# Kernel tuning notes

Hardware: AMD Instinct MI355X
Metric: run time of the kernel (lower is better)

## Reference

```python
import jax, jax.numpy as jnp
import numpy as np

B = 512        # number of graphs
NPG = 128      # nodes per graph
N = B * NPG    # total nodes = 65536
E = 262144     # total edges (intra-graph)
F_IN = 128     # input features
H = 256        # hidden
C = 2          # num classes
BN_EPS = 1e-5


def _lin_params(key, fan_in, fan_out):
    k1, k2 = jax.random.split(key)
    s = 1.0 / np.sqrt(fan_in)
    w = jax.random.uniform(k1, (fan_in, fan_out), jnp.float32, -s, s)
    b = jax.random.uniform(k2, (fan_out,), jnp.float32, -s, s)
    return w, b


def setup_inputs() -> dict:
    key = jax.random.key(0)
    ks = jax.random.split(key, 16)
    x = jax.random.normal(ks[0], (N, F_IN), jnp.float32)
    # intra-graph random edges (required for assignment pooling semantics)
    rng = np.random.RandomState(0)
    g = np.repeat(np.arange(B), E // B)
    src = g * NPG + rng.randint(0, NPG, E)
    dst = g * NPG + rng.randint(0, NPG, E)
    edge_index = jnp.asarray(np.stack([src, dst]), jnp.int64 if jax.config.jax_enable_x64 else jnp.int32)
    batch = jnp.repeat(jnp.arange(B), NPG)
    # GIN layer 0 (F_IN->H->H) + BN
    w0_1, b0_1 = _lin_params(ks[1], F_IN, H)
    w0_2, b0_2 = _lin_params(ks[2], H, H)
    g0 = jnp.ones((H,), jnp.float32); be0 = jnp.zeros((H,), jnp.float32)
    # GIN layers 1..2 stacked (H->H->H) + BN
    wl1 = jnp.stack([_lin_params(jax.random.fold_in(ks[3], i), H, H)[0] for i in range(2)])
    bl1 = jnp.stack([_lin_params(jax.random.fold_in(ks[3], i), H, H)[1] for i in range(2)])
    wl2 = jnp.stack([_lin_params(jax.random.fold_in(ks[4], i), H, H)[0] for i in range(2)])
    bl2 = jnp.stack([_lin_params(jax.random.fold_in(ks[4], i), H, H)[1] for i in range(2)])
    gl = jnp.ones((2, H), jnp.float32); bel = jnp.zeros((2, H), jnp.float32)
    c1w, c1b = _lin_params(ks[5], H, H)
    c2w, c2b = _lin_params(ks[6], H, 2)
    l1w, l1b = _lin_params(ks[7], H, H)
    l2w, l2b = _lin_params(ks[8], H, C)
    return dict(x=x, edge_index=edge_index, batch=batch,
                w0_1=w0_1, b0_1=b0_1, w0_2=w0_2, b0_2=b0_2, g0=g0, be0=be0,
                wl1=wl1, bl1=bl1, wl2=wl2, bl2=bl2, gl=gl, bel=bel,
                c1w=c1w, c1b=c1b, c2w=c2w, c2b=c2b,
                l1w=l1w, l1b=l1b, l2w=l2w, l2b=l2b)


def _gin_layer(h, src, dst, w1, b1, w2, b2, gamma, beta):
    # GINConv (eps=0): MLP(h + sum_{j in N(i)} h_j)
    agg = jax.ops.segment_sum(h[src], dst, num_segments=N)
    z = h + agg
    z = jax.nn.relu(z @ w1 + b1)
    z = jax.nn.relu(z @ w2 + b2)
    # BatchNorm1d, training-mode batch stats (biased variance)
    mu = jnp.mean(z, axis=0)
    var = jnp.mean((z - mu) ** 2, axis=0)
    return (z - mu) * jax.lax.rsqrt(var + BN_EPS) * gamma + beta


def reference(x, edge_index, batch, w0_1, b0_1, w0_2, b0_2, g0, be0,
              wl1, bl1, wl2, bl2, gl, bel,
              c1w, c1b, c2w, c2b, l1w, l1b, l2w, l2b):
    src, dst = edge_index[0], edge_index[1]
    h = _gin_layer(x, src, dst, w0_1, b0_1, w0_2, b0_2, g0, be0)
    for i in range(2):
        h = _gin_layer(h, src, dst, wl1[i], bl1[i], wl2[i], bl2[i], gl[i], bel[i])
    # assignment: softmax(cluster2(tanh(cluster1(h))))  -> [N, 2]
    a = jax.nn.softmax(jnp.tanh(h @ c1w + c1b) @ c2w + c2b, axis=1)
    # subgraph embedding: (assignment^T @ x)[0] per graph == segment-sum of a[:,0]*h
    sub = jax.ops.segment_sum(a[:, :1] * h, batch, num_segments=B)        # [B, H]
    # graph embedding: per-graph mean of h
    cnt = jax.ops.segment_sum(jnp.ones((N,), h.dtype), batch, num_segments=B)
    graph = jax.ops.segment_sum(h, batch, num_segments=B) / cnt[:, None]   # [B, H]
    # new_adj[g] = A_g^T-pooled: sum over edges outer(a[src], a[dst]) -> [B,2,2]
    new_adj = jax.ops.segment_sum(a[src][:, :, None] * a[dst][:, None, :], batch[src], num_segments=B)
    # F.normalize(p=1, dim=1) row-wise, then diagonal, MSE vs ones(2)
    rown = jnp.maximum(jnp.sum(jnp.abs(new_adj), axis=2, keepdims=True), 1e-12)
    norm_adj = new_adj / rown
    diag = jnp.diagonal(norm_adj, axis1=1, axis2=2)                        # [B, 2]
    con_penalty = jnp.mean(jnp.mean((diag - 1.0) ** 2, axis=1))
    # classifier head (dropout in eval mode -> identity)
    z = jax.nn.relu(sub @ l1w + l1b)
    out = jax.nn.log_softmax(z @ l2w + l2b, axis=-1)
    return out, sub, graph, con_penalty
```

## Files before the change

### kernel.cpp

```cpp
#include <hip/hip_runtime.h>
#include <stdint.h>

#define NN 65536
#define NB 512
#define NPG 128
#define NE 262144
#define EPG 512
#define HD 256
#define BN_EPS 1e-5f

typedef unsigned short u16;
typedef float f32x4 __attribute__((ext_vector_type(4)));
typedef __bf16 bf16x8 __attribute__((ext_vector_type(8)));
typedef unsigned short u16x8 __attribute__((ext_vector_type(8)));
typedef unsigned short u16x4 __attribute__((ext_vector_type(4)));

__device__ __forceinline__ float b2f(u16 u){
  union { unsigned i; float f; } x; x.i = ((unsigned)u) << 16; return x.f;
}
__device__ __forceinline__ u16 f2b(float f){
  union { float f; unsigned i; } x; x.f = f;
  unsigned r = x.i + 0x7fffu + ((x.i >> 16) & 1u);
  return (u16)(r >> 16);
}

__global__ void __launch_bounds__(256) pack_all(
    const float* __restrict__ w0_1, const float* __restrict__ w0_2,
    const float* __restrict__ wl1, const float* __restrict__ wl2,
    const float* __restrict__ c1w,
    u16* i01, u16* i02, u16* il1a, u16* il1b, u16* il2a, u16* il2b, u16* ic1)
{
  const int seg = blockIdx.y;
  const int idx = blockIdx.x * 256 + threadIdx.x;
  const float* W; u16* img; int K = 256;
  switch (seg){
    case 0: W = w0_1;        img = i01;  K = 128; break;
    case 1: W = w0_2;        img = i02;  break;
    case 2: W = wl1;         img = il1a; break;
    case 3: W = wl1 + 65536; img = il1b; break;
    case 4: W = wl2;         img = il2a; break;
    case 5: W = wl2 + 65536; img = il2b; break;
    default: W = c1w;        img = ic1;  break;
  }
  if (idx >= K * 256) return;
  int col = idx / K, k = idx - col * K;
  img[idx] = f2b(W[(size_t)k * 256 + col]);
}

template<int K>
__device__ __forceinline__ void mm_frag(const u16* Alds,
    const u16* __restrict__ wimg, int lane, int c0, f32x4 (&acc)[8][2])
{
  const int l15 = lane & 15, lk = (lane >> 4) * 8;
  bf16x8 bfr[K / 32][2];
  #pragma unroll
  for (int kk = 0; kk < K / 32; kk++)
    #pragma unroll
    for (int nf = 0; nf < 2; nf++)
      bfr[kk][nf] = *(const bf16x8*)(wimg + (size_t)(c0 + nf * 16 + l15) * K + kk * 32 + lk);
  #pragma unroll
  for (int kk = 0; kk < K / 32; kk++){
    bf16x8 af[8];
    #pragma unroll
    for (int mf = 0; mf < 8; mf++){
      int row = mf * 16 + l15;
      unsigned byte = ((unsigned)(row * (K * 2) + (kk * 32 + lk) * 2)) ^ (unsigned)((row & 7) << 4);
      af[mf] = *(const bf16x8*)((const char*)Alds + byte);
    }
    #pragma unroll
    for (int mf = 0; mf < 8; mf++)
      #pragma unroll
      for (int nf = 0; nf < 2; nf++)
        acc[mf][nf] = __builtin_amdgcn_mfma_f32_16x16x32_bf16(af[mf], bfr[kk][nf], acc[mf][nf], 0, 0, 0);
  }
}

template<int KIN, int MODE>
__global__ void __launch_bounds__(512) layer_kernel(
    const void* __restrict__ hin_, const int* __restrict__ ei,
    const float* __restrict__ sc, const float* __restrict__ sh,
    const u16* __restrict__ w1img, const float* __restrict__ b1,
    const u16* __restrict__ w2img, const float* __restrict__ b2,
    u16* __restrict__ Y, float* __restrict__ pS, float* __restrict__ pQ)
{
  __shared__ u16 ht[NPG * KIN];
  __shared__ u16 z1[NPG * HD];
  __shared__ int es[EPG], ed[EPG], srcs[EPG];
  __shared__ int cnt[NPG], rp[NPG + 1], fill[NPG];
  __shared__ float scs[256], shs[256];
  const int g = blockIdx.x, tid = threadIdx.x;
  const int lane = tid & 63, wid = tid >> 6;

  if (tid < NPG) cnt[tid] = 0;
  if (MODE == 1 && tid < 256){ scs[tid] = sc[tid]; shs[tid] = sh[tid]; }
  __syncthreads();

  {
    int s = ei[g * EPG + tid] & (NPG - 1);
    int d = ei[NE + g * EPG + tid] & (NPG - 1);
    es[tid] = s; ed[tid] = d;
    atomicAdd(&cnt[d], 1);
  }

  if constexpr (MODE == 0){
    const float* hin = (const float*)hin_;
    #pragma unroll
    for (int i = 0; i < 8; i++){
      int idx = tid + i * 512;
      int row = idx >> 5, c4 = idx & 31;
      float4 v = *(const float4*)(hin + (size_t)(g * NPG + row) * KIN + c4 * 4);
      u16x4 o; o[0] = f2b(v.x); o[1] = f2b(v.y); o[2] = f2b(v.z); o[3] = f2b(v.w);
      unsigned byte = ((unsigned)(row * (KIN * 2) + c4 * 8)) ^ (unsigned)((row & 7) << 4);
      *(u16x4*)((char*)ht + byte) = o;
    }
  } else {
    const u16* hin = (const u16*)hin_;
    #pragma unroll
    for (int i = 0; i < 8; i++){
      int idx = tid + i * 512;
      int row = idx >> 5, c8 = idx & 31;
      u16x8 v = *(const u16x8*)(hin + (size_t)(g * NPG + row) * KIN + c8 * 8);
      u16x8 o;
      #pragma unroll
      for (int k = 0; k < 8; k++) o[k] = f2b(b2f(v[k]) * scs[c8 * 8 + k] + shs[c8 * 8 + k]);
      unsigned byte = ((unsigned)(row * (KIN * 2) + c8 * 16)) ^ (unsigned)((row & 7) << 4);
      *(u16x8*)((char*)ht + byte) = o;
    }
  }
  __syncthreads();

  if (tid < 64){
    int a = cnt[tid], b = cnt[tid + 64];
    int ca = a, cb = b;
    #pragma unroll
    for (int off = 1; off < 64; off <<= 1){
      int ta = __shfl_up(a, off), tb = __shfl_up(b, off);
      if (lane >= off){ a += ta; b += tb; }
    }
    int atot = __shfl(a, 63);
    rp[tid + 1] = a;
    rp[tid + 65] = atot + b;
    fill[tid] = a - ca;
    fill[tid + 64] = atot + b - cb;
    if (tid == 0) rp[0] = 0;
  }
  __syncthreads();
  { int pos = atomicAdd(&fill[ed[tid]], 1); srcs[pos] = es[tid]; }
  __syncthreads();

  constexpr int CH = KIN / 16;
  constexpr int RPT = NPG * CH / 512;
  const int fc = tid & (CH - 1), n0 = tid / CH;
  float accv[RPT][16];
  #pragma unroll
  for (int j = 0; j < RPT; j++){
    const int n = n0 + j * (512 / CH);
    unsigned b0 = ((unsigned)(n * (KIN * 2) + fc * 32)) ^ (unsigned)((n & 7) << 4);
    u16x8 a0 = *(const u16x8*)((const char*)ht + b0);
    u16x8 a1 = *(const u16x8*)((const char*)ht + (b0 ^ 16u));
    #pragma unroll
    for (int k = 0; k < 8; k++){ accv[j][k] = b2f(a0[k]); accv[j][8 + k] = b2f(a1[k]); }
    const int e0 = rp[n], e1 = rp[n + 1];
    for (int e = e0; e < e1; e++){
      const int sn = srcs[e];
      unsigned s0 = ((unsigned)(sn * (KIN * 2) + fc * 32)) ^ (unsigned)((sn & 7) << 4);
      u16x8 q0 = *(const u16x8*)((const char*)ht + s0);
      u16x8 q1 = *(const u16x8*)((const char*)ht + (s0 ^ 16u));
      #pragma unroll
      for (int k = 0; k < 8; k++){ accv[j][k] += b2f(q0[k]); accv[j][8 + k] += b2f(q1[k]); }
    }
  }
  __syncthreads();
  #pragma unroll
  for (int j = 0; j < RPT; j++){
    const int n = n0 + j * (512 / CH);
    u16x8 o0, o1;
    #pragma unroll
    for (int k = 0; k < 8; k++){ o0[k] = f2b(accv[j][k]); o1[k] = f2b(accv[j][8 + k]); }
    unsigned b0 = ((unsigned)(n * (KIN * 2) + fc * 32)) ^ (unsigned)((n & 7) << 4);
    *(u16x8*)((char*)ht + b0) = o0;
    *(u16x8*)((char*)ht + (b0 ^ 16u)) = o1;
  }
  __syncthreads();

  const int c0 = wid * 32;
  const int l15 = lane & 15;
  {
    f32x4 acc1[8][2] = {};
    mm_frag<KIN>(ht, w1img, lane, c0, acc1);
    float bv0 = b1[c0 + l15], bv1 = b1[c0 + 16 + l15];
    #pragma unroll
    for (int mf = 0; mf < 8; mf++)
      #pragma unroll
      for (int nf = 0; nf < 2; nf++){
        float bv = nf ? bv1 : bv0;
        int col = c0 + nf * 16 + l15;
        #pragma unroll
        for (int j = 0; j < 4; j++){
          int row = mf * 16 + (lane >> 4) * 4 + j;
          float v = fmaxf(acc1[mf][nf][j] + bv, 0.f);
          unsigned byte = ((unsigned)(row * 512 + col * 2)) ^ (unsigned)((row & 7) << 4);
          *(u16*)((char*)z1 + byte) = f2b(v);
        }
      }
  }
  __syncthreads();

  {
    f32x4 acc2[8][2] = {};
    mm_frag<HD>(z1, w2img, lane, c0, acc2);
    float bv0 = b2[c0 + l15], bv1 = b2[c0 + 16 + l15];
    float s[2] = {0, 0}, q[2] = {0, 0};
    #pragma unroll
    for (int mf = 0; mf < 8; mf++)
      #pragma unroll
      for (int nf = 0; nf < 2; nf++){
        float bv = nf ? bv1 : bv0;
        int col = c0 + nf * 16 + l15;
        #pragma unroll
        for (int j = 0; j < 4; j++){
          int row = mf * 16 + (lane >> 4) * 4 + j;
          float v = fmaxf(acc2[mf][nf][j] + bv, 0.f);
          Y[(size_t)(g * NPG + row) * HD + col] = f2b(v);
          s[nf] += v; q[nf] += v * v;
        }
      }
    #pragma unroll
    for (int nf = 0; nf < 2; nf++){
      float sv = s[nf], qv = q[nf];
      sv += __shfl_xor(sv, 16); sv += __shfl_xor(sv, 32);
      qv += __shfl_xor(qv, 16); qv += __shfl_xor(qv, 32);
      if (lane < 16){
        int col = c0 + nf * 16 + lane;
        pS[(size_t)col * NB + g] = sv;
        pQ[(size_t)col * NB + g] = qv;
      }
    }
  }
}

__global__ void __launch_bounds__(64) bnfin_kernel(const float* __restrict__ pS,
    const float* __restrict__ pQ, const float* __restrict__ gma,
    const float* __restrict__ bta, float* __restrict__ scale, float* __restrict__ shift)
{
  int c = blockIdx.x, lane = threadIdx.x;
  float s = 0.f, q = 0.f;
  for (int i = lane; i < NB; i += 64){ s += pS[(size_t)c * NB + i]; q += pQ[(size_t)c * NB + i]; }
  for (int m = 32; m; m >>= 1){ s += __shfl_xor(s, m); q += __shfl_xor(q, m); }
  if (lane == 0){
    float mu = s * (1.0f / NN);
    float var = q * (1.0f / NN) - mu * mu;
    float scv = gma[c] * rsqrtf(var + BN_EPS);
    scale[c] = scv;
    shift[c] = bta[c] - mu * scv;
  }
}

__global__ void __launch_bounds__(512) final_kernel(
    const u16* __restrict__ hin, const int* __restrict__ ei,
    const float* __restrict__ sc, const float* __restrict__ sh,
    const u16* __restrict__ c1img, const float* __restrict__ c1b,
    const float* __restrict__ c2w, const float* __restrict__ c2b,
    const float* __restrict__ l1w, const float* __restrict__ l1b,
    const float* __restrict__ l2w, const float* __restrict__ l2b,
    float* __restrict__ outLog, float* __restrict__ outSub,
    float* __restrict__ outGraph, float* __restrict__ pg)
{
  __shared__ u16 ht[NPG * HD];
  __shared__ u16 tt[NPG * HD];
  __shared__ int es[EPG], ed[EPG];
  __shared__ float aL[NPG * 2];
  __shared__ float c2ws[512];
  __shared__ float scs[256], shs[256];
  __shared__ float red2[1024];
  __shared__ float subL[256];
  __shared__ float wred[8][4];
  const int g = blockIdx.x, tid = threadIdx.x;
  const int lane = tid & 63, wid = tid >> 6;

  if (tid < 256){ scs[tid] = sc[tid]; shs[tid] = sh[tid]; }
  c2ws[tid] = c2w[tid];
  es[tid] = ei[g * EPG + tid] & (NPG - 1);
  ed[tid] = ei[NE + g * EPG + tid] & (NPG - 1);
  __syncthreads();

  #pragma unroll
  for (int i = 0; i < 8; i++){
    int idx = tid + i * 512;
    int row = idx >> 5, c8 = idx & 31;
    u16x8 v = *(const u16x8*)(hin + (size_t)(g * NPG + row) * HD + c8 * 8);
    u16x8 o;
    #pragma unroll
    for (int k = 0; k < 8; k++) o[k] = f2b(b2f(v[k]) * scs[c8 * 8 + k] + shs[c8 * 8 + k]);
    unsigned byte = ((unsigned)(row * 512 + c8 * 16)) ^ (unsigned)((row & 7) << 4);
    *(u16x8*)((char*)ht + byte) = o;
  }
  __syncthreads();

  const int c0 = wid * 32;
  const int l15 = lane & 15;
  {
    f32x4 acct[8][2] = {};
    mm_frag<HD>(ht, c1img, lane, c0, acct);
    float bv0 = c1b[c0 + l15], bv1 = c1b[c0 + 16 + l15];
    #pragma unroll
    for (int mf = 0; mf < 8; mf++)
      #pragma unroll
      for (int nf = 0; nf < 2; nf++){
        float bv = nf ? bv1 : bv0;
        int col = c0 + nf * 16 + l15;
        #pragma unroll
        for (int j = 0; j < 4; j++){
          int row = mf * 16 + (lane >> 4) * 4 + j;
          tt[row * HD + col] = f2b(tanhf(acct[mf][nf][j] + bv));
        }
      }
  }
  __syncthreads();

  {
    const int n = tid >> 2, qd = tid & 3;
    float s0 = 0.f, s1 = 0.f;
    #pragma unroll
    for (int i = 0; i < 8; i++){
      u16x8 v = *(const u16x8*)&tt[n * HD + qd * 64 + i * 8];
      #pragma unroll
      for (int k = 0; k < 8; k++){
        float f = b2f(v[k]); int col = qd * 64 + i * 8 + k;
        s0 += f * c2ws[col * 2]; s1 += f * c2ws[col * 2 + 1];
      }
    }
    s0 += __shfl_xor(s0, 1); s0 += __shfl_xor(s0, 2);
    s1 += __shfl_xor(s1, 1); s1 += __shfl_xor(s1, 2);
    if (qd == 0){
      s0 += c2b[0]; s1 += c2b[1];
      float mx = fmaxf(s0, s1);
      float e0 = expf(s0 - mx), e1 = expf(s1 - mx);
      float inv = 1.f / (e0 + e1);
      aL[n * 2] = e0 * inv; aL[n * 2 + 1] = e1 * inv;
    }
  }
  __syncthreads();

  {
    float as0 = aL[es[tid] * 2], as1 = aL[es[tid] * 2 + 1];
    float ad0 = aL[ed[tid] * 2], ad1 = aL[ed[tid] * 2 + 1];
    float m00 = as0 * ad0, m01 = as0 * ad1, m10 = as1 * ad0, m11 = as1 * ad1;
    #pragma unroll
    for (int m = 1; m < 64; m <<= 1){
      m00 += __shfl_xor(m00, m); m01 += __shfl_xor(m01, m);
      m10 += __shfl_xor(m10, m); m11 += __shfl_xor(m11, m);
    }
    if (lane == 0){ wred[wid][0] = m00; wred[wid][1] = m01; wred[wid][2] = m10; wred[wid][3] = m11; }
  }
  {
    const int part = tid >> 8, c = tid & 255;
    float sb = 0.f, gs = 0.f;
    #pragma unroll 8
    for (int i = 0; i < 64; i++){
      int n = part * 64 + i;
      unsigned byte = ((unsigned)(n * 512 + c * 2)) ^ (unsigned)((n & 7) << 4);
      float v = b2f(*(const u16*)((const char*)ht + byte));
      sb += aL[n * 2] * v; gs += v;
    }
    red2[part * 512 + c] = sb;
    red2[part * 512 + 256 + c] = gs;
  }
  __syncthreads();
  if (tid < 256){
    float sb = red2[tid] + red2[512 + tid];
    float gs = red2[256 + tid] + red2[768 + tid];
    subL[tid] = sb;
    outSub[(size_t)g * HD + tid] = sb;
    outGraph[(size_t)g * HD + tid] = gs * (1.f / NPG);
  }
  if (tid == 0){
    float m00 = 0, m01 = 0, m10 = 0, m11 = 0;
    for (int w = 0; w < 8; w++){ m00 += wred[w][0]; m01 += wred[w][1]; m10 += wred[w][2]; m11 += wred[w][3]; }
    float r0 = fmaxf(fabsf(m00) + fabsf(m01), 1e-12f);
    float r1 = fmaxf(fabsf(m10) + fabsf(m11), 1e-12f);
    float d0 = m00 / r0 - 1.f, d1 = m11 / r1 - 1.f;
    pg[g] = 0.5f * (d0 * d0 + d1 * d1);
  }
  __syncthreads();

  {
    const int ph = tid >> 8, c = tid & 255;
    float z = 0.f;
    for (int k = ph * 128; k < ph * 128 + 128; k++)
      z += subL[k] * l1w[(size_t)k * HD + c];
    red2[ph * 256 + c] = z;
  }
  __syncthreads();
  if (tid < 256){
    float z = fmaxf(red2[tid] + red2[256 + tid] + l1b[tid], 0.f);
    float o0 = z * l2w[tid * 2], o1 = z * l2w[tid * 2 + 1];
    #pragma unroll
    for (int m = 1; m < 64; m <<= 1){ o0 += __shfl_xor(o0, m); o1 += __shfl_xor(o1, m); }
    if (lane == 0){ wred[wid][0] = o0; wred[wid][1] = o1; }
  }
  __syncthreads();
  if (tid == 0){
    float o0 = wred[0][0] + wred[1][0] + wred[2][0] + wred[3][0] + l2b[0];
    float o1 = wred[0][1] + wred[1][1] + wred[2][1] + wred[3][1] + l2b[1];
    float mx = fmaxf(o0, o1);
    float lse = mx + logf(expf(o0 - mx) + expf(o1 - mx));
    outLog[(size_t)g * 2] = o0 - lse;
    outLog[(size_t)g * 2 + 1] = o1 - lse;
  }
}

__global__ void __launch_bounds__(256) penred_kernel(const float* __restrict__ pg,
                                                     float* __restrict__ outPen)
{
  const int tid = threadIdx.x;
  float s = pg[tid] + pg[tid + 256];
  for (int m = 32; m; m >>= 1) s += __shfl_xor(s, m);
  __shared__ float wsum[4];
  if ((tid & 63) == 0) wsum[tid >> 6] = s;
  __syncthreads();
  if (tid == 0) outPen[0] = (wsum[0] + wsum[1] + wsum[2] + wsum[3]) * (1.0f / NB);
}

extern "C" void kernel_launch(void* const* d_in, const int* in_sizes, int n_in,
                              void* d_out, int out_size, void* d_ws, size_t ws_size,
                              hipStream_t stream)
{
  (void)in_sizes; (void)n_in; (void)out_size; (void)ws_size;
  const float* x    = (const float*)d_in[0];
  const int*   ei   = (const int*)  d_in[1];
  const float* w0_1 = (const float*)d_in[3];
  const float* b0_1 = (const float*)d_in[4];
  const float* w0_2 = (const float*)d_in[5];
  const float* b0_2 = (const float*)d_in[6];
  const float* g0   = (const float*)d_in[7];
  const float* be0  = (const float*)d_in[8];
  const float* wl1  = (const float*)d_in[9];
  const float* bl1  = (const float*)d_in[10];
  const float* wl2  = (const float*)d_in[11];
  const float* bl2  = (const float*)d_in[12];
  const float* gl   = (const float*)d_in[13];
  const float* bel  = (const float*)d_in[14];
  const float* c1w  = (const float*)d_in[15];
  const float* c1b  = (const float*)d_in[16];
  const float* c2w  = (const float*)d_in[17];
  const float* c2b  = (const float*)d_in[18];
  const float* l1w  = (const float*)d_in[19];
  const float* l1b  = (const float*)d_in[20];
  const float* l2w  = (const float*)d_in[21];
  const float* l2b  = (const float*)d_in[22];
  float* out = (float*)d_out;

  char* cur = (char*)d_ws;
  auto carve = [&](size_t bytes) -> void* {
    void* p = (void*)cur; cur += (bytes + 255) & ~(size_t)255; return p;
  };
  u16* B0    = (u16*)carve((size_t)NN * HD * 2);
  u16* B1    = (u16*)carve((size_t)NN * HD * 2);
  u16* i01   = (u16*)carve((size_t)128 * 256 * 2);
  u16* i02   = (u16*)carve((size_t)256 * 256 * 2);
  u16* il1a  = (u16*)carve((size_t)256 * 256 * 2);
  u16* il1b  = (u16*)carve((size_t)256 * 256 * 2);
  u16* il2a  = (u16*)carve((size_t)256 * 256 * 2);
  u16* il2b  = (u16*)carve((size_t)256 * 256 * 2);
  u16* ic1   = (u16*)carve((size_t)256 * 256 * 2);
  float* pS  = (float*)carve((size_t)256 * NB * 4);
  float* pQ  = (float*)carve((size_t)256 * NB * 4);
  float* bsc = (float*)carve(256 * 4);
  float* bsh = (float*)carve(256 * 4);
  float* pg  = (float*)carve(NB * 4);

  pack_all<<<dim3(256, 7), 256, 0, stream>>>(w0_1, w0_2, wl1, wl2, c1w,
                                             i01, i02, il1a, il1b, il2a, il2b, ic1);

  layer_kernel<128, 0><<<NB, 512, 0, stream>>>((const void*)x, ei, nullptr, nullptr,
                                               i01, b0_1, i02, b0_2, B0, pS, pQ);
  bnfin_kernel<<<256, 64, 0, stream>>>(pS, pQ, g0, be0, bsc, bsh);

  layer_kernel<256, 1><<<NB, 512, 0, stream>>>((const void*)B0, ei, bsc, bsh,
                                               il1a, bl1, il2a, bl2, B1, pS, pQ);
  bnfin_kernel<<<256, 64, 0, stream>>>(pS, pQ, gl, bel, bsc, bsh);

  layer_kernel<256, 1><<<NB, 512, 0, stream>>>((const void*)B1, ei, bsc, bsh,
                                               il1b, bl1 + 256, il2b, bl2 + 256, B0, pS, pQ);
  bnfin_kernel<<<256, 64, 0, stream>>>(pS, pQ, gl + 256, bel + 256, bsc, bsh);

  final_kernel<<<NB, 512, 0, stream>>>(B0, ei, bsc, bsh, ic1, c1b, c2w, c2b,
                                       l1w, l1b, l2w, l2b,
                                       out, out + 1024, out + 1024 + NB * HD, pg);
  penred_kernel<<<1, 256, 0, stream>>>(pg, out + 1024 + 2 * NB * HD);
}
```

Before: 309.4 us.

## Cut shared memory in layer and final kernels, fuse cluster head, drop penalty kernel

The layer kernel now reuses the ht buffer for the first MLP output instead of a separate z1 buffer, and packs source and destination edge indices into 16-bit values. Together these shrink LDS use per block so more blocks can be resident per CU. The final kernel fuses the tanh and c2 projection into the MFMA epilogue using a fast exp-based tanh and lane shuffles, which removes the tt buffer and folds the small scratch arrays into one. The separate penalty-reduction kernel is replaced by a float atomicAdd after a memset. The cost is an extra barrier, a less accurate tanh, and a penalty sum whose order is nondeterministic.

```diff
diff --git a/kernel.cpp b/kernel.cpp
--- a/kernel.cpp
+++ b/kernel.cpp
@@ -22,6 +22,10 @@
   union { float f; unsigned i; } x; x.f = f;
   unsigned r = x.i + 0x7fffu + ((x.i >> 16) & 1u);
   return (u16)(r >> 16);
+}
+__device__ __forceinline__ float ftanh(float x){
+  float e = __expf(2.0f * x);
+  return 1.0f - 2.0f * __builtin_amdgcn_rcpf(e + 1.0f);
 }
 
 __global__ void __launch_bounds__(256) pack_all(
@@ -83,9 +87,9 @@
     const u16* __restrict__ w2img, const float* __restrict__ b2,
     u16* __restrict__ Y, float* __restrict__ pS, float* __restrict__ pQ)
 {
-  __shared__ u16 ht[NPG * KIN];
-  __shared__ u16 z1[NPG * HD];
-  __shared__ int es[EPG], ed[EPG], srcs[EPG];
+  __shared__ u16 ht[NPG * HD];
+  __shared__ u16 esd[EPG];
+  __shared__ u16 srcs[EPG];
   __shared__ int cnt[NPG], rp[NPG + 1], fill[NPG];
   __shared__ float scs[256], shs[256];
   const int g = blockIdx.x, tid = threadIdx.x;
@@ -98,7 +102,7 @@
   {
     int s = ei[g * EPG + tid] & (NPG - 1);
     int d = ei[NE + g * EPG + tid] & (NPG - 1);
-    es[tid] = s; ed[tid] = d;
+    esd[tid] = (u16)(s | (d << 8));
     atomicAdd(&cnt[d], 1);
   }
 
@@ -145,7 +149,7 @@
     if (tid == 0) rp[0] = 0;
   }
   __syncthreads();
-  { int pos = atomicAdd(&fill[ed[tid]], 1); srcs[pos] = es[tid]; }
+  { int v = esd[tid]; int pos = atomicAdd(&fill[v >> 8], 1); srcs[pos] = (u16)(v & 255); }
   __syncthreads();
 
   constexpr int CH = KIN / 16;
@@ -185,9 +189,11 @@
 
   const int c0 = wid * 32;
   const int l15 = lane & 15;
+
   {
     f32x4 acc1[8][2] = {};
     mm_frag<KIN>(ht, w1img, lane, c0, acc1);
+    __syncthreads();
     float bv0 = b1[c0 + l15], bv1 = b1[c0 + 16 + l15];
     #pragma unroll
     for (int mf = 0; mf < 8; mf++)
@@ -200,7 +206,7 @@
           int row = mf * 16 + (lane >> 4) * 4 + j;
           float v = fmaxf(acc1[mf][nf][j] + bv, 0.f);
           unsigned byte = ((unsigned)(row * 512 + col * 2)) ^ (unsigned)((row & 7) << 4);
-          *(u16*)((char*)z1 + byte) = f2b(v);
+          *(u16*)((char*)ht + byte) = f2b(v);
         }
       }
   }
@@ -208,7 +214,7 @@
 
   {
     f32x4 acc2[8][2] = {};
-    mm_frag<HD>(z1, w2img, lane, c0, acc2);
+    mm_frag<HD>(ht, w2img, lane, c0, acc2);
     float bv0 = b2[c0 + l15], bv1 = b2[c0 + 16 + l15];
     float s[2] = {0, 0}, q[2] = {0, 0};
     #pragma unroll
@@ -264,24 +270,23 @@
     const float* __restrict__ l1w, const float* __restrict__ l1b,
     const float* __restrict__ l2w, const float* __restrict__ l2b,
     float* __restrict__ outLog, float* __restrict__ outSub,
-    float* __restrict__ outGraph, float* __restrict__ pg)
+    float* __restrict__ outGraph, float* __restrict__ outPen)
 {
   __shared__ u16 ht[NPG * HD];
-  __shared__ u16 tt[NPG * HD];
-  __shared__ int es[EPG], ed[EPG];
+  __shared__ u16 esd[EPG];
   __shared__ float aL[NPG * 2];
-  __shared__ float c2ws[512];
-  __shared__ float scs[256], shs[256];
-  __shared__ float red2[1024];
+  __shared__ float scratch[2048];
   __shared__ float subL[256];
   __shared__ float wred[8][4];
   const int g = blockIdx.x, tid = threadIdx.x;
   const int lane = tid & 63, wid = tid >> 6;
 
-  if (tid < 256){ scs[tid] = sc[tid]; shs[tid] = sh[tid]; }
-  c2ws[tid] = c2w[tid];
-  es[tid] = ei[g * EPG + tid] & (NPG - 1);
-  ed[tid] = ei[NE + g * EPG + tid] & (NPG - 1);
+  if (tid < 256){ scratch[tid] = sc[tid]; scratch[256 + tid] = sh[tid]; }
+  {
+    int s = ei[g * EPG + tid] & (NPG - 1);
+    int d = ei[NE + g * EPG + tid] & (NPG - 1);
+    esd[tid] = (u16)(s | (d << 8));
+  }
   __syncthreads();
 
   #pragma unroll
@@ -291,7 +296,8 @@
     u16x8 v = *(const u16x8*)(hin + (size_t)(g * NPG + row) * HD + c8 * 8);
     u16x8 o;
     #pragma unroll
-    for (int k = 0; k < 8; k++) o[k] = f2b(b2f(v[k]) * scs[c8 * 8 + k] + shs[c8 * 8 + k]);
+    for (int k = 0; k < 8; k++)
+      o[k] = f2b(b2f(v[k]) * scratch[c8 * 8 + k] + scratch[256 + c8 * 8 + k]);
     unsigned byte = ((unsigned)(row * 512 + c8 * 16)) ^ (unsigned)((row & 7) << 4);
     *(u16x8*)((char*)ht + byte) = o;
   }
@@ -299,52 +305,56 @@
 
   const int c0 = wid * 32;
   const int l15 = lane & 15;
+
   {
     f32x4 acct[8][2] = {};
     mm_frag<HD>(ht, c1img, lane, c0, acct);
-    float bv0 = c1b[c0 + l15], bv1 = c1b[c0 + 16 + l15];
+    const int col0 = c0 + l15, col1 = c0 + 16 + l15;
+    const float bv0 = c1b[col0], bv1 = c1b[col1];
+    const float w00 = c2w[col0 * 2], w01 = c2w[col0 * 2 + 1];
+    const float w10 = c2w[col1 * 2], w11 = c2w[col1 * 2 + 1];
     #pragma unroll
     for (int mf = 0; mf < 8; mf++)
       #pragma unroll
-      for (int nf = 0; nf < 2; nf++){
-        float bv = nf ? bv1 : bv0;
-        int col = c0 + nf * 16 + l15;
-        #pragma unroll
-        for (int j = 0; j < 4; j++){
+      for (int j = 0; j < 4; j++){
+        float t0 = ftanh(acct[mf][0][j] + bv0);
+        float t1 = ftanh(acct[mf][1][j] + bv1);
+        float p0 = t0 * w00 + t1 * w10;
+        float p1 = t0 * w01 + t1 * w11;
+        p0 += __shfl_xor(p0, 1); p0 += __shfl_xor(p0, 2);
+        p0 += __shfl_xor(p0, 4); p0 += __shfl_xor(p0, 8);
+        p1 += __shfl_xor(p1, 1); p1 += __shfl_xor(p1, 2);
+        p1 += __shfl_xor(p1, 4); p1 += __shfl_xor(p1, 8);
+        if (l15 == 0){
           int row = mf * 16 + (lane >> 4) * 4 + j;
-          tt[row * HD + col] = f2b(tanhf(acct[mf][nf][j] + bv));
+          scratch[row * 16 + wid * 2]     = p0;
+          scratch[row * 16 + wid * 2 + 1] = p1;
         }
       }
   }
   __syncthreads();
 
   {
-    const int n = tid >> 2, qd = tid & 3;
-    float s0 = 0.f, s1 = 0.f;
-    #pragma unroll
-    for (int i = 0; i < 8; i++){
-      u16x8 v = *(const u16x8*)&tt[n * HD + qd * 64 + i * 8];
-      #pragma unroll
-      for (int k = 0; k < 8; k++){
-        float f = b2f(v[k]); int col = qd * 64 + i * 8 + k;
-        s0 += f * c2ws[col * 2]; s1 += f * c2ws[col * 2 + 1];
-      }
-    }
-    s0 += __shfl_xor(s0, 1); s0 += __shfl_xor(s0, 2);
-    s1 += __shfl_xor(s1, 1); s1 += __shfl_xor(s1, 2);
-    if (qd == 0){
-      s0 += c2b[0]; s1 += c2b[1];
-      float mx = fmaxf(s0, s1);
-      float e0 = expf(s0 - mx), e1 = expf(s1 - mx);
+    int row = tid >> 2, part = tid & 3;
+    float4 v = *(const float4*)&scratch[row * 16 + part * 4];
+    float p0 = v.x + v.z, p1 = v.y + v.w;
+    p0 += __shfl_xor(p0, 1); p0 += __shfl_xor(p0, 2);
+    p1 += __shfl_xor(p1, 1); p1 += __shfl_xor(p1, 2);
+    if (part == 0){
+      p0 += c2b[0]; p1 += c2b[1];
+      float mx = fmaxf(p0, p1);
+      float e0 = expf(p0 - mx), e1 = expf(p1 - mx);
       float inv = 1.f / (e0 + e1);
-      aL[n * 2] = e0 * inv; aL[n * 2 + 1] = e1 * inv;
-    }
-  }
-  __syncthreads();
-
-  {
-    float as0 = aL[es[tid] * 2], as1 = aL[es[tid] * 2 + 1];
-    float ad0 = aL[ed[tid] * 2], ad1 = aL[ed[tid] * 2 + 1];
+      aL[row * 2] = e0 * inv; aL[row * 2 + 1] = e1 * inv;
+    }
+  }
+  __syncthreads();
+
+  {
+    int v = esd[tid];
+    int sE = v & 255, dE = v >> 8;
+    float as0 = aL[sE * 2], as1 = aL[sE * 2 + 1];
+    float ad0 = aL[dE * 2], ad1 = aL[dE * 2 + 1];
     float m00 = as0 * ad0, m01 = as0 * ad1, m10 = as1 * ad0, m11 = as1 * ad1;
     #pragma unroll
     for (int m = 1; m < 64; m <<= 1){
@@ -363,13 +373,14 @@
       float v = b2f(*(const u16*)((const char*)ht + byte));
       sb += aL[n * 2] * v; gs += v;
     }
-    red2[part * 512 + c] = sb;
-    red2[part * 512 + 256 + c] = gs;
+    __syncthreads();
+    scratch[part * 512 + c] = sb;
+    scratch[part * 512 + 256 + c] = gs;
   }
   __syncthreads();
   if (tid < 256){
-    float sb = red2[tid] + red2[512 + tid];
-    float gs = red2[256 + tid] + red2[768 + tid];
+    float sb = scratch[tid] + scratch[512 + tid];
+    float gs = scratch[256 + tid] + scratch[768 + tid];
     subL[tid] = sb;
     outSub[(size_t)g * HD + tid] = sb;
     outGraph[(size_t)g * HD + tid] = gs * (1.f / NPG);
@@ -380,7 +391,7 @@
     float r0 = fmaxf(fabsf(m00) + fabsf(m01), 1e-12f);
     float r1 = fmaxf(fabsf(m10) + fabsf(m11), 1e-12f);
     float d0 = m00 / r0 - 1.f, d1 = m11 / r1 - 1.f;
-    pg[g] = 0.5f * (d0 * d0 + d1 * d1);
+    atomicAdd(outPen, 0.5f * (d0 * d0 + d1 * d1) * (1.0f / NB));
   }
   __syncthreads();
 
@@ -389,11 +400,11 @@
     float z = 0.f;
     for (int k = ph * 128; k < ph * 128 + 128; k++)
       z += subL[k] * l1w[(size_t)k * HD + c];
-    red2[ph * 256 + c] = z;
+    scratch[ph * 256 + c] = z;
   }
   __syncthreads();
   if (tid < 256){
-    float z = fmaxf(red2[tid] + red2[256 + tid] + l1b[tid], 0.f);
+    float z = fmaxf(scratch[tid] + scratch[256 + tid] + l1b[tid], 0.f);
     float o0 = z * l2w[tid * 2], o1 = z * l2w[tid * 2 + 1];
     #pragma unroll
     for (int m = 1; m < 64; m <<= 1){ o0 += __shfl_xor(o0, m); o1 += __shfl_xor(o1, m); }
@@ -408,18 +419,6 @@
     outLog[(size_t)g * 2] = o0 - lse;
     outLog[(size_t)g * 2 + 1] = o1 - lse;
   }
-}
-
-__global__ void __launch_bounds__(256) penred_kernel(const float* __restrict__ pg,
-                                                     float* __restrict__ outPen)
-{
-  const int tid = threadIdx.x;
-  float s = pg[tid] + pg[tid + 256];
-  for (int m = 32; m; m >>= 1) s += __shfl_xor(s, m);
-  __shared__ float wsum[4];
-  if ((tid & 63) == 0) wsum[tid >> 6] = s;
-  __syncthreads();
-  if (tid == 0) outPen[0] = (wsum[0] + wsum[1] + wsum[2] + wsum[3]) * (1.0f / NB);
 }
 
 extern "C" void kernel_launch(void* const* d_in, const int* in_sizes, int n_in,
@@ -468,10 +467,12 @@
   float* pQ  = (float*)carve((size_t)256 * NB * 4);
   float* bsc = (float*)carve(256 * 4);
   float* bsh = (float*)carve(256 * 4);
-  float* pg  = (float*)carve(NB * 4);
+
+  float* outPen = out + 1024 + 2 * NB * HD;
 
   pack_all<<<dim3(256, 7), 256, 0, stream>>>(w0_1, w0_2, wl1, wl2, c1w,
                                              i01, i02, il1a, il1b, il2a, il2b, ic1);
+  hipMemsetAsync((void*)outPen, 0, 4, stream);
 
   layer_kernel<128, 0><<<NB, 512, 0, stream>>>((const void*)x, ei, nullptr, nullptr,
                                                i01, b0_1, i02, b0_2, B0, pS, pQ);
@@ -487,6 +488,5 @@
 
   final_kernel<<<NB, 512, 0, stream>>>(B0, ei, bsc, bsh, ic1, c1b, c2w, c2b,
                                        l1w, l1b, l2w, l2b,
-                                       out, out + 1024, out + 1024 + NB * HD, pg);
-  penred_kernel<<<1, 256, 0, stream>>>(pg, out + 1024 + 2 * NB * HD);
-}
+                                       out, out + 1024, out + 1024 + NB * HD, outPen);
+}
```

Result: faster. 288.2 us (-6.9%).
